# Performance work log

Measured on AMD Instinct MI355X. Metric: run time of the kernel, lower is better.

The kernel has to match this reference:

```python
import jax, jax.numpy as jnp
import numpy as np

NUM_CAPS = 2          # NUM_CLASSES
R = 16 * 10 * 10 * 10 # num_route_nodes = 16000
NUM_ITERS = 3


def conv3d(x, w, b, stride):
    y = jax.lax.conv_general_dilated(
        x, w, window_strides=(stride, stride, stride), padding='VALID',
        dimension_numbers=('NCDHW', 'OIDHW', 'NCDHW'))
    return y + b[None, :, None, None, None]


def squash(t, axis=-1):
    n = jnp.linalg.norm(t, axis=axis, keepdims=True)
    scale = n ** 2 / (1 + n ** 2) / (n + 1e-8)
    return scale * t


def setup_inputs() -> dict:
    key = jax.random.key(0)
    ks = jax.random.split(key, 16)
    inp = {
        'x': jax.random.normal(ks[0], (16, 1, 29, 29, 29), jnp.float32),
        'conv1_w': 0.05 * jax.random.normal(ks[1], (128, 1, 3, 3, 3), jnp.float32),
        'conv1_b': jnp.zeros((128,), jnp.float32),
        # 8 primary capsules, each Conv3d(128,16,k=9,s=2), stacked cap-major
        'pcaps_w': 0.01 * jax.random.normal(ks[2], (8 * 16, 128, 9, 9, 9), jnp.float32),
        'pcaps_b': jnp.zeros((8 * 16,), jnp.float32),
        'route_w': 0.01 * jax.random.normal(ks[3], (NUM_CAPS, R, 8, 16), jnp.float32),
        'dec_w1': 0.05 * jax.random.normal(ks[4], (32, 512), jnp.float32),
        'dec_b1': jnp.zeros((512,), jnp.float32),
        'dec_w2': 0.05 * jax.random.normal(ks[5], (512, 2048), jnp.float32),
        'dec_b2': jnp.zeros((2048,), jnp.float32),
        'dec_w3': 0.02 * jax.random.normal(ks[6], (2048, 10240), jnp.float32),
        'dec_b3': jnp.zeros((10240,), jnp.float32),
        'dec_w4': 0.02 * jax.random.normal(ks[7], (10240, 27000), jnp.float32),
        'dec_b4': jnp.zeros((27000,), jnp.float32),
    }
    return inp


def reference(x, conv1_w, conv1_b, pcaps_w, pcaps_b, route_w,
              dec_w1, dec_b1, dec_w2, dec_b2, dec_w3, dec_b3, dec_w4, dec_b4):
    B = x.shape[0]
    # stem conv + relu: [B,128,27,27,27]
    h = jax.nn.relu(conv3d(x, conv1_w, conv1_b, 1))
    # primary capsules (8 convs fused into one): [B,128,10,10,10]
    p = conv3d(h, pcaps_w, pcaps_b, 2)
    # torch: per-capsule view(B,-1,1) then cat dim=-1 -> [B,16000,8]
    p = p.reshape(B, 8, R).transpose(0, 2, 1)
    u = squash(p, axis=-1)  # [B,R,8]

    # priors: x[:,None,:,None,:] @ W[None] -> [B,C,R,16] (singleton dim dropped)
    priors = jnp.einsum('bri,crio->bcro', u, route_w)
    priors_d = jax.lax.stop_gradient(priors)
    # torch logits have trailing dim 16 but are constant along it (delta is
    # broadcast), so [B,C,R,1] is mathematically identical.
    logits = jnp.zeros((B, NUM_CAPS, R, 1), priors.dtype)

    for i in range(NUM_ITERS):
        probs = jax.nn.softmax(logits, axis=1)  # over capsule axis
        if i == NUM_ITERS - 1:
            v = squash((probs * priors).sum(axis=2, keepdims=True))
        else:
            v = squash((probs * priors_d).sum(axis=2, keepdims=True))
            logits = logits + (priors_d * v).sum(axis=-1, keepdims=True)

    caps = v[:, :, 0, :]  # [B,C,16] (squeeze)
    classes = jnp.linalg.norm(caps, axis=-1)  # [B,C]

    # y=None branch: one-hot of argmax
    y = jax.nn.one_hot(jnp.argmax(classes, axis=1), NUM_CAPS, dtype=caps.dtype)
    d = (caps * y[:, :, None]).reshape(B, -1)  # [B,32]
    d = jax.nn.relu(d @ dec_w1 + dec_b1)
    d = jax.nn.relu(d @ dec_w2 + dec_b2)
    d = jax.nn.relu(d @ dec_w3 + dec_b3)
    recon = jax.nn.sigmoid(d @ dec_w4 + dec_b4)  # [B,27000]
    return classes, recon
```

## Files before the change

kernel.cpp:

```cpp
#include <hip/hip_runtime.h>
#include <hip/hip_bf16.h>

#define NB   16
#define XS   29
#define HS   27
#define HSP  19683
#define PSP  1000
#define RR   16000
#define KTAP 729
#define SPTOT 314928

#define HT_SLOT   81648UL
#define HT_TOTAL  41803776UL
#define HT_PLANE  3024
#define W2B_CH    4096
#define W2B_ICG   376832UL

#define OFF_WT   0UL
#define OFF_H    11943936UL
#define OFF_SP   52254720UL
#define OFF_U    54302720UL
#define OFF_PRI  56350720UL
#define OFF_LOG  64542720UL
#define OFF_V    65055232UL
#define OFF_D0   65055744UL
#define OFF_D1   65056256UL
#define OFF_D2   65064448UL
#define OFF_D3   65097216UL
#define OFF_PP   65693056UL
#define OFF_D3P  82077056UL
#define OFF_D4P  84698496UL

typedef __attribute__((ext_vector_type(8))) short bf16x8;
typedef __attribute__((ext_vector_type(4))) float f32x4;

#define GL2LDS16(g, l) __builtin_amdgcn_global_load_lds( \
    (const __attribute__((address_space(1))) void*)(g), \
    (__attribute__((address_space(3))) void*)(l), 16, 0, 0)

__global__ void prep_w2b(const float* __restrict__ w, ushort* __restrict__ w2b) {
    int gid = blockIdx.x * 256 + threadIdx.x;
    int oc  = gid / 11776;
    int r   = gid % 11776;
    int icg = r / 368;
    int r2  = r % 368;
    int c = r2 >> 2, kq = r2 & 3;
    const float* wb = w + (size_t)oc * 93312 + (size_t)icg * 4 * KTAP;
    ushort vals[8];
    #pragma unroll
    for (int j = 0; j < 8; j++) {
        int ic = j & 3, half = j >> 2;
        float v = 0.f;
        if (c < 81) {
            int tap = c * 9 + 2 * kq + half;
            v = wb[ic * KTAP + tap];
        } else {
            int dzy = (c - 81) * 8 + 2 * kq + half;
            if (dzy <= 80) v = wb[ic * KTAP + dzy * 9 + 8];
        }
        __hip_bfloat16 hv = __float2bfloat16(v);
        vals[j] = *(ushort*)&hv;
    }
    ushort* dst = w2b + ((size_t)((icg * 92 + c) * 4 + kq) * 128 + oc) * 8;
    #pragma unroll
    for (int j = 0; j < 8; j++) dst[j] = vals[j];
}

__global__ __launch_bounds__(256) void conv1_relu_t(const float* __restrict__ x,
                                                    const float* __restrict__ w,
                                                    const float* __restrict__ bias,
                                                    ushort* __restrict__ hT) {
    __shared__ ushort lt[32][132];
    int t = threadIdx.x;
    int c = t & 127;
    float wr[27];
    #pragma unroll
    for (int k = 0; k < 27; k++) wr[k] = w[c * 27 + k];
    float bv = bias[c];
    int sp0 = blockIdx.x * 32;
    #pragma unroll 4
    for (int i = 0; i < 16; i++) {
        int spl = i * 2 + (t >> 7);
        int spg = sp0 + spl;
        if (spg < SPTOT) {
            int b = spg / HSP, sp = spg % HSP;
            int z = sp / 729, y = (sp / 27) % 27, xx = sp % 27;
            const float* xb = x + (size_t)b * (XS * XS * XS) + ((size_t)z * XS + y) * XS + xx;
            float xv[27];
            #pragma unroll
            for (int dz = 0; dz < 3; dz++)
                #pragma unroll
                for (int dy = 0; dy < 3; dy++)
                    #pragma unroll
                    for (int dx = 0; dx < 3; dx++)
                        xv[(dz * 3 + dy) * 3 + dx] = xb[((size_t)dz * XS + dy) * XS + dx];
            float acc = bv;
            #pragma unroll
            for (int k = 0; k < 27; k++) acc = fmaf(xv[k], wr[k], acc);
            __hip_bfloat16 hv = __float2bfloat16(fmaxf(acc, 0.f));
            lt[spl][c] = *(ushort*)&hv;
        }
    }
    __syncthreads();
    #pragma unroll
    for (int q = 0; q < 4; q++) {
        int gidx = q * 256 + t;
        int icg = gidx >> 5, spl = gidx & 31;
        int spg = sp0 + spl;
        if (spg < SPTOT) {
            int b = spg / HSP, sp = spg % HSP;
            int z = sp / 729, y = (sp / 27) % 27, xx = sp % 27;
            *(short4*)(hT + (size_t)(icg * 16 + b) * HT_SLOT
                          + ((size_t)(z * 27 + y) * 28 + xx) * 4) =
                *(const short4*)&lt[spl][icg * 4];
        }
    }
}

__global__ __launch_bounds__(512, 4) void pcaps_conv(const ushort* __restrict__ hT,
                                                     const ushort* __restrict__ w2b,
                                                     float* __restrict__ pp) {
    __shared__ __align__(16) ushort AT[36288];
    int t = threadIdx.x;
    int bid = blockIdx.x;
    int g = bid & 7;
    int rest = bid >> 3;
    int b = rest / 5, ozt = rest % 5;
    int z0 = ozt * 4;

    int lane = t & 63, wave = t >> 6;
    int ocb = wave * 16;
    int l15 = lane & 15, kq = lane >> 4;

    int vox[13];
    #pragma unroll
    for (int f = 0; f < 13; f++) {
        int lr = f * 16 + l15; if (lr > 199) lr = 199;
        int ozl = lr / 100; int rem = lr % 100;
        int oy = rem / 10, ox = rem % 10;
        vox[f] = (2 * ozl) * 6048 + (2 * oy) * 224 + (2 * ox) * 8;
    }

    f32x4 acc[13];
    #pragma unroll
    for (int f = 0; f < 13; f++) acc[f] = (f32x4)0.f;

    int bvoff = (kq * 128 + ocb + l15) * 8;

    for (int ph = 0; ph < 4; ++ph) {
        int icg = g * 4 + ph;
        const ushort* src = hT + (size_t)(icg * 16 + b) * HT_SLOT + (size_t)z0 * HT_PLANE;
        if (ph) __syncthreads();
        #pragma unroll
        for (int q = 0; q < 9; q++) {
            int gi = q * 512 + t;
            if (gi < 4536)
                GL2LDS16(src + (size_t)gi * 8, AT + (size_t)gi * 8);
        }
        asm volatile("s_waitcnt vmcnt(0)" ::: "memory");
        __syncthreads();

        const ushort* wB = w2b + (size_t)icg * W2B_ICG;
        bf16x8 bv = *(const bf16x8*)(wB + bvoff);
        for (int c = 0; c < 81; ++c) {
            bf16x8 bvn = *(const bf16x8*)(wB + (size_t)(c + 1) * W2B_CH + bvoff);
            int coff = (c / 9) * 6048 + (c % 9) * 224 + kq * 16;
            #pragma unroll
            for (int f = 0; f < 13; f++) {
                bf16x8 av = *(const bf16x8*)((const char*)AT + vox[f] + coff);
                acc[f] = __builtin_amdgcn_mfma_f32_16x16x32_bf16(av, bv, acc[f], 0, 0, 0);
            }
            bv = bvn;
        }
        for (int cc = 0; cc < 11; ++cc) {
            int nxt = (cc == 10) ? 91 : 82 + cc;
            bf16x8 bvn = *(const bf16x8*)(wB + (size_t)nxt * W2B_CH + bvoff);
            int dzy0 = cc * 8 + 2 * kq;
            int dzy1 = dzy0 + 1;
            int o0 = (dzy0 / 9) * 6048 + (dzy0 % 9) * 224 + 64;
            int o1 = (dzy1 / 9) * 6048 + (dzy1 % 9) * 224 + 64;
            #pragma unroll
            for (int f = 0; f < 13; f++) {
                union { bf16x8 v; short4 h[2]; } a;
                a.h[0] = *(const short4*)((const char*)AT + vox[f] + o0);
                a.h[1] = *(const short4*)((const char*)AT + vox[f] + o1);
                acc[f] = __builtin_amdgcn_mfma_f32_16x16x32_bf16(a.v, bv, acc[f], 0, 0, 0);
            }
            bv = bvn;
        }
    }

    float* pg = pp + (size_t)g * 2048000;
    int mbase = b * 1000 + ozt * 200;
    #pragma unroll
    for (int f = 0; f < 13; f++) {
        #pragma unroll
        for (int r = 0; r < 4; r++) {
            int lr = f * 16 + kq * 4 + r;
            if (lr < 200)
                pg[(size_t)(mbase + lr) * 128 + ocb + l15] = acc[f][r];
        }
    }
}

__global__ void squash_red(const float* __restrict__ pp, const float* __restrict__ pb,
                           float* __restrict__ u) {
    __shared__ float rowv[2][128];
    int t = threadIdx.x;
    int m = blockIdx.x * 2 + (t >> 7);
    int ch = t & 127;
    float v = pb[ch];
    #pragma unroll
    for (int g = 0; g < 8; g++) v += pp[(size_t)g * 2048000 + (size_t)m * 128 + ch];
    rowv[t >> 7][ch] = v;
    __syncthreads();
    if (t < 32) {
        int row = t >> 4, rq = t & 15;
        int mm = blockIdx.x * 2 + row;
        int b = mm / PSP, s = mm % PSP;
        float vals[8], ss = 0.f;
        #pragma unroll
        for (int i = 0; i < 8; i++) { float x = rowv[row][i * 16 + rq]; vals[i] = x; ss += x * x; }
        float n = sqrtf(ss);
        float sc = ss / (1.f + ss) / (n + 1e-8f);
        float* dst = u + ((size_t)b * RR + rq * 1000 + s) * 8;
        #pragma unroll
        for (int i = 0; i < 8; i++) dst[i] = vals[i] * sc;
    }
}

__global__ void priors_k(const float* __restrict__ u, const float* __restrict__ rw,
                         float* __restrict__ pri) {
    __shared__ float wl[16][132];
    int bx = blockIdx.x; int c = bx / 1000; int r0 = (bx % 1000) * 16;
    int t = threadIdx.x;
    const float4* src = (const float4*)(rw + ((size_t)c * RR + r0) * 128);
    #pragma unroll
    for (int q = 0; q < 8; q++) {
        int idx = q * 256 + t;
        int row = idx >> 5, c4 = idx & 31;
        *(float4*)&wl[row][c4 * 4] = src[idx];
    }
    __syncthreads();
    int bb = t >> 4, rl = t & 15;
    const float* up = u + ((size_t)bb * RR + r0 + rl) * 8;
    float4 u0 = *(const float4*)up, u1 = *(const float4*)(up + 4);
    float uu[8] = {u0.x, u0.y, u0.z, u0.w, u1.x, u1.y, u1.z, u1.w};
    float out[16];
    #pragma unroll
    for (int o = 0; o < 16; o++) out[o] = 0.f;
    #pragma unroll
    for (int i = 0; i < 8; i++)
        #pragma unroll
        for (int o = 0; o < 16; o++) out[o] += uu[i] * wl[rl][i * 16 + o];
    float* dst = pri + ((size_t)(bb * 2 + c) * RR + r0 + rl) * 16;
    #pragma unroll
    for (int q = 0; q < 4; q++)
        *(float4*)&dst[q * 4] = make_float4(out[q*4], out[q*4+1], out[q*4+2], out[q*4+3]);
}

__global__ void route_s0(const float* __restrict__ pri, float* __restrict__ spart) {
    int b = blockIdx.x, chunk = blockIdx.y;
    int t = threadIdx.x, o = t & 15, rl = t >> 4;
    float acc0 = 0.f, acc1 = 0.f;
    for (int j = 0; j < 40; j++) {
        int r = chunk * 640 + j * 16 + rl;
        acc0 += pri[((size_t)(b * 2 + 0) * RR + r) * 16 + o];
        acc1 += pri[((size_t)(b * 2 + 1) * RR + r) * 16 + o];
    }
    __shared__ float red[2][16][17];
    red[0][rl][o] = acc0; red[1][rl][o] = acc1;
    __syncthreads();
    for (int step = 8; step >= 1; step >>= 1) {
        if (rl < step) {
            red[0][rl][o] += red[0][rl + step][o];
            red[1][rl][o] += red[1][rl + step][o];
        }
        __syncthreads();
    }
    if (rl == 0) {
        spart[((b * 25 + chunk) * 2 + 0) * 16 + o] = 0.5f * red[0][0][o];
        spart[((b * 25 + chunk) * 2 + 1) * 16 + o] = 0.5f * red[1][0][o];
    }
}

template<int MODE>
__global__ void route_iter(const float* __restrict__ pri, const float* __restrict__ v,
                           float* __restrict__ lg, float* __restrict__ spart) {
    int b = blockIdx.x, chunk = blockIdx.y;
    int t = threadIdx.x, o = t & 15, rl = t >> 4;
    float v0 = v[(b * 2 + 0) * 16 + o], v1 = v[(b * 2 + 1) * 16 + o];
    float acc0 = 0.f, acc1 = 0.f;
    for (int j = 0; j < 40; j++) {
        int r = chunk * 640 + j * 16 + rl;
        float p0 = pri[((size_t)(b * 2 + 0) * RR + r) * 16 + o];
        float p1 = pri[((size_t)(b * 2 + 1) * RR + r) * 16 + o];
        float d0 = p0 * v0, d1 = p1 * v1;
        #pragma unroll
        for (int w = 1; w < 16; w <<= 1) { d0 += __shfl_xor(d0, w); d1 += __shfl_xor(d1, w); }
        float l0, l1;
        if (MODE == 1) {
            l0 = d0; l1 = d1;
            if (o == 0) lg[(size_t)(b * 2 + 0) * RR + r] = d0;
            if (o == 1) lg[(size_t)(b * 2 + 1) * RR + r] = d1;
        } else {
            l0 = lg[(size_t)(b * 2 + 0) * RR + r] + d0;
            l1 = lg[(size_t)(b * 2 + 1) * RR + r] + d1;
        }
        float mx = fmaxf(l0, l1);
        float e0 = __expf(l0 - mx), e1 = __expf(l1 - mx);
        float inv = 1.f / (e0 + e1);
        acc0 += (e0 * inv) * p0;
        acc1 += (e1 * inv) * p1;
    }
    __shared__ float red[2][16][17];
    red[0][rl][o] = acc0; red[1][rl][o] = acc1;
    __syncthreads();
    for (int step = 8; step >= 1; step >>= 1) {
        if (rl < step) {
            red[0][rl][o] += red[0][rl + step][o];
            red[1][rl][o] += red[1][rl + step][o];
        }
        __syncthreads();
    }
    if (rl == 0) {
        spart[((b * 25 + chunk) * 2 + 0) * 16 + o] = red[0][0][o];
        spart[((b * 25 + chunk) * 2 + 1) * 16 + o] = red[1][0][o];
    }
}

__global__ void squash_v_parts(const float* __restrict__ spart, float* __restrict__ v) {
    int t = threadIdx.x;
    int bc = t >> 4, o = t & 15;
    int b = bc >> 1, c = bc & 1;
    float x = 0.f;
    for (int ch = 0; ch < 25; ch++) x += spart[((b * 25 + ch) * 2 + c) * 16 + o];
    __shared__ float sv[32][17];
    sv[bc][o] = x;
    __syncthreads();
    float ss = 0.f;
    #pragma unroll
    for (int i = 0; i < 16; i++) { float y = sv[bc][i]; ss += y * y; }
    float n = sqrtf(ss);
    float sc = ss / (1.f + ss) / (n + 1e-8f);
    v[bc * 16 + o] = x * sc;
}

__global__ void squash_v_cls(const float* __restrict__ spart, float* __restrict__ out,
                             float* __restrict__ d0) {
    int t = threadIdx.x;
    int bc = t >> 4, o = t & 15;
    int b = bc >> 1, c = bc & 1;
    float x = 0.f;
    for (int ch = 0; ch < 25; ch++) x += spart[((b * 25 + ch) * 2 + c) * 16 + o];
    __shared__ float sv[32][17];
    __shared__ float vv[32][17];
    __shared__ float cls[32];
    sv[bc][o] = x;
    __syncthreads();
    float ss = 0.f;
    #pragma unroll
    for (int i = 0; i < 16; i++) { float y = sv[bc][i]; ss += y * y; }
    float n = sqrtf(ss);
    float sc = ss / (1.f + ss) / (n + 1e-8f);
    vv[bc][o] = x * sc;
    __syncthreads();
    if (t < 32) {
        float s2 = 0.f;
        #pragma unroll
        for (int i = 0; i < 16; i++) { float y = vv[t][i]; s2 += y * y; }
        float nn = sqrtf(s2);
        cls[t] = nn; out[t] = nn;
    }
    __syncthreads();
    int bb = t >> 5, k = t & 31, cc = k >> 4;
    int win = (cls[bb * 2 + 1] > cls[bb * 2 + 0]) ? 1 : 0;
    d0[t] = (cc == win) ? vv[bb * 2 + cc][k & 15] : 0.f;
}

template<int K>
__global__ void dec_small(const float* __restrict__ din, const float* __restrict__ W,
                          const float* __restrict__ bias, float* __restrict__ dout, int N) {
    __shared__ float dl[16 * K];
    int t = threadIdx.x;
    for (int i = t; i < 16 * K; i += 256) dl[i] = din[i];
    __syncthreads();
    int n = blockIdx.x * 256 + t;
    if (n >= N) return;
    float acc[16];
    float bv = bias[n];
    #pragma unroll
    for (int b = 0; b < 16; b++) acc[b] = bv;
    for (int k = 0; k < K; k++) {
        float w = W[(size_t)k * N + n];
        #pragma unroll
        for (int b = 0; b < 16; b++) acc[b] += dl[b * K + k] * w;
    }
    #pragma unroll
    for (int b = 0; b < 16; b++) dout[(size_t)b * N + n] = fmaxf(acc[b], 0.f);
}

__global__ void dec_split(const float* __restrict__ din, const float* __restrict__ W,
                          float* __restrict__ part, int N, int K, int KC) {
    extern __shared__ float dl[];
    int t = threadIdx.x;
    int ky = blockIdx.y;
    int k0 = ky * KC;
    for (int i = t; i < 16 * KC; i += 256) {
        int b = i / KC, kk = i % KC;
        dl[i] = din[(size_t)b * K + k0 + kk];
    }
    __syncthreads();
    int n = blockIdx.x * 1024 + t * 4;
    if (n >= N) return;
    float4 acc[16];
    #pragma unroll
    for (int b = 0; b < 16; b++) acc[b] = make_float4(0.f, 0.f, 0.f, 0.f);
    const float* Wp = W + (size_t)k0 * N + n;
    for (int kk = 0; kk < KC; kk++) {
        float4 w = *(const float4*)&Wp[(size_t)kk * N];
        #pragma unroll
        for (int b = 0; b < 16; b++) {
            float dv = dl[b * KC + kk];
            acc[b].x += dv * w.x; acc[b].y += dv * w.y;
            acc[b].z += dv * w.z; acc[b].w += dv * w.w;
        }
    }
    #pragma unroll
    for (int b = 0; b < 16; b++)
        *(float4*)&part[((size_t)(ky * 16 + b)) * N + n] = acc[b];
}

__global__ void bias_act_sum(const float* __restrict__ part, const float* __restrict__ bias,
                             float* __restrict__ out, int N, int total, int sigm) {
    int gid = blockIdx.x * 256 + threadIdx.x;
    if (gid >= total) return;
    int b = gid / N, n = gid % N;
    float x = bias[n];
    #pragma unroll
    for (int ky = 0; ky < 16; ky++)
        x += part[((size_t)(ky * 16 + b)) * N + n];
    out[gid] = sigm ? (1.f / (1.f + __expf(-x))) : fmaxf(x, 0.f);
}

extern "C" void kernel_launch(void* const* d_in, const int* in_sizes, int n_in,
                              void* d_out, int out_size, void* d_ws, size_t ws_size,
                              hipStream_t stream) {
    const float* x        = (const float*)d_in[0];
    const float* conv1_w  = (const float*)d_in[1];
    const float* conv1_b  = (const float*)d_in[2];
    const float* pcaps_w  = (const float*)d_in[3];
    const float* pcaps_b  = (const float*)d_in[4];
    const float* route_w  = (const float*)d_in[5];
    const float* dec_w1   = (const float*)d_in[6];
    const float* dec_b1   = (const float*)d_in[7];
    const float* dec_w2   = (const float*)d_in[8];
    const float* dec_b2   = (const float*)d_in[9];
    const float* dec_w3   = (const float*)d_in[10];
    const float* dec_b3   = (const float*)d_in[11];
    const float* dec_w4   = (const float*)d_in[12];
    const float* dec_b4   = (const float*)d_in[13];
    float* out = (float*)d_out;

    float* ws = (float*)d_ws;
    ushort* w2b = (ushort*)(ws + OFF_WT);
    ushort* hT  = (ushort*)(ws + OFF_H);
    float* spart = ws + OFF_SP;
    float* u    = ws + OFF_U;
    float* pri  = ws + OFF_PRI;
    float* lg   = ws + OFF_LOG;
    float* v    = ws + OFF_V;
    float* d0   = ws + OFF_D0;
    float* d1   = ws + OFF_D1;
    float* d2   = ws + OFF_D2;
    float* d3   = ws + OFF_D3;
    float* pp   = ws + OFF_PP;
    float* d3p  = ws + OFF_D3P;
    float* d4p  = ws + OFF_D4P;

    prep_w2b<<<5888, 256, 0, stream>>>(pcaps_w, w2b);
    conv1_relu_t<<<9842, 256, 0, stream>>>(x, conv1_w, conv1_b, hT);
    hipMemsetAsync(hT + HT_TOTAL, 0, 8192, stream);

    pcaps_conv<<<640, 512, 0, stream>>>(hT, w2b, pp);
    squash_red<<<8000, 256, 0, stream>>>(pp, pcaps_b, u);

    priors_k<<<2000, 256, 0, stream>>>(u, route_w, pri);

    route_s0<<<dim3(16, 25), 256, 0, stream>>>(pri, spart);
    squash_v_parts<<<1, 512, 0, stream>>>(spart, v);
    route_iter<1><<<dim3(16, 25), 256, 0, stream>>>(pri, v, lg, spart);
    squash_v_parts<<<1, 512, 0, stream>>>(spart, v);
    route_iter<2><<<dim3(16, 25), 256, 0, stream>>>(pri, v, lg, spart);
    squash_v_cls<<<1, 512, 0, stream>>>(spart, out, d0);

    dec_small<32><<<2, 256, 0, stream>>>(d0, dec_w1, dec_b1, d1, 512);
    dec_small<512><<<8, 256, 0, stream>>>(d1, dec_w2, dec_b2, d2, 2048);

    dec_split<<<dim3(10, 16), 256, 16 * 128 * sizeof(float), stream>>>(d2, dec_w3, d3p, 10240, 2048, 128);
    bias_act_sum<<<(16 * 10240 + 255) / 256, 256, 0, stream>>>(d3p, dec_b3, d3, 10240, 16 * 10240, 0);

    dec_split<<<dim3(27, 16), 256, 16 * 640 * sizeof(float), stream>>>(d3, dec_w4, d4p, 27000, 10240, 640);
    bias_act_sum<<<(16 * 27000 + 255) / 256, 256, 0, stream>>>(d4p, dec_b4, out + 32, 27000, 16 * 27000, 1);
}
```

Measured before the change: 1.215 ms.

## Retile pcaps conv waves to 2x32 output tiles and deepen decoder split-K

The primary-capsule conv now gives each wave 32 output channels over half the voxel rows, so every A fragment loaded from LDS feeds two MFMAs. This halves LDS reads per MFMA, though the second B fragment adds extra global weight loads. Separately, the two large decoder GEMMs split K into 32 and 64 chunks instead of 16 to launch more blocks and use more CUs. That makes the partial buffers larger, so the workspace offset is moved and the reduction kernel now takes a variable count of partials.

```diff
diff --git a/kernel.cpp b/kernel.cpp
--- a/kernel.cpp
+++ b/kernel.cpp
@@ -29,7 +29,7 @@
 #define OFF_D3   65097216UL
 #define OFF_PP   65693056UL
 #define OFF_D3P  82077056UL
-#define OFF_D4P  84698496UL
+#define OFF_D4P  87319936UL
 
 typedef __attribute__((ext_vector_type(8))) short bf16x8;
 typedef __attribute__((ext_vector_type(4))) float f32x4;
@@ -129,23 +129,24 @@
     int z0 = ozt * 4;
 
     int lane = t & 63, wave = t >> 6;
-    int ocb = wave * 16;
+    int wo = wave & 3, wm = wave >> 2;
+    int ocb = wo * 32;
     int l15 = lane & 15, kq = lane >> 4;
 
-    int vox[13];
-    #pragma unroll
-    for (int f = 0; f < 13; f++) {
-        int lr = f * 16 + l15; if (lr > 199) lr = 199;
-        int ozl = lr / 100; int rem = lr % 100;
-        int oy = rem / 10, ox = rem % 10;
-        vox[f] = (2 * ozl) * 6048 + (2 * oy) * 224 + (2 * ox) * 8;
-    }
-
-    f32x4 acc[13];
-    #pragma unroll
-    for (int f = 0; f < 13; f++) acc[f] = (f32x4)0.f;
-
-    int bvoff = (kq * 128 + ocb + l15) * 8;
+    int vox[7];
+    #pragma unroll
+    for (int f = 0; f < 7; f++) {
+        int lr = f * 16 + l15; if (lr > 99) lr = 99;
+        int oy = lr / 10, ox = lr % 10;
+        vox[f] = (2 * wm) * 6048 + (2 * oy) * 224 + (2 * ox) * 8;
+    }
+
+    f32x4 acc[7][2];
+    #pragma unroll
+    for (int f = 0; f < 7; f++) { acc[f][0] = (f32x4)0.f; acc[f][1] = (f32x4)0.f; }
+
+    int bvoff0 = (kq * 128 + ocb + l15) * 8;
+    int bvoff1 = bvoff0 + 128;
 
     for (int ph = 0; ph < 4; ++ph) {
         int icg = g * 4 + ph;
@@ -161,44 +162,52 @@
         __syncthreads();
 
         const ushort* wB = w2b + (size_t)icg * W2B_ICG;
-        bf16x8 bv = *(const bf16x8*)(wB + bvoff);
+        bf16x8 bv0 = *(const bf16x8*)(wB + bvoff0);
+        bf16x8 bv1 = *(const bf16x8*)(wB + bvoff1);
         for (int c = 0; c < 81; ++c) {
-            bf16x8 bvn = *(const bf16x8*)(wB + (size_t)(c + 1) * W2B_CH + bvoff);
+            bf16x8 bn0 = *(const bf16x8*)(wB + (size_t)(c + 1) * W2B_CH + bvoff0);
+            bf16x8 bn1 = *(const bf16x8*)(wB + (size_t)(c + 1) * W2B_CH + bvoff1);
             int coff = (c / 9) * 6048 + (c % 9) * 224 + kq * 16;
             #pragma unroll
-            for (int f = 0; f < 13; f++) {
+            for (int f = 0; f < 7; f++) {
                 bf16x8 av = *(const bf16x8*)((const char*)AT + vox[f] + coff);
-                acc[f] = __builtin_amdgcn_mfma_f32_16x16x32_bf16(av, bv, acc[f], 0, 0, 0);
+                acc[f][0] = __builtin_amdgcn_mfma_f32_16x16x32_bf16(av, bv0, acc[f][0], 0, 0, 0);
+                acc[f][1] = __builtin_amdgcn_mfma_f32_16x16x32_bf16(av, bv1, acc[f][1], 0, 0, 0);
             }
-            bv = bvn;
+            bv0 = bn0; bv1 = bn1;
         }
         for (int cc = 0; cc < 11; ++cc) {
             int nxt = (cc == 10) ? 91 : 82 + cc;
-            bf16x8 bvn = *(const bf16x8*)(wB + (size_t)nxt * W2B_CH + bvoff);
+            bf16x8 bn0 = *(const bf16x8*)(wB + (size_t)nxt * W2B_CH + bvoff0);
+            bf16x8 bn1 = *(const bf16x8*)(wB + (size_t)nxt * W2B_CH + bvoff1);
             int dzy0 = cc * 8 + 2 * kq;
             int dzy1 = dzy0 + 1;
             int o0 = (dzy0 / 9) * 6048 + (dzy0 % 9) * 224 + 64;
             int o1 = (dzy1 / 9) * 6048 + (dzy1 % 9) * 224 + 64;
             #pragma unroll
-            for (int f = 0; f < 13; f++) {
+            for (int f = 0; f < 7; f++) {
                 union { bf16x8 v; short4 h[2]; } a;
                 a.h[0] = *(const short4*)((const char*)AT + vox[f] + o0);
                 a.h[1] = *(const short4*)((const char*)AT + vox[f] + o1);
-                acc[f] = __builtin_amdgcn_mfma_f32_16x16x32_bf16(a.v, bv, acc[f], 0, 0, 0);
+                acc[f][0] = __builtin_amdgcn_mfma_f32_16x16x32_bf16(a.v, bv0, acc[f][0], 0, 0, 0);
+                acc[f][1] = __builtin_amdgcn_mfma_f32_16x16x32_bf16(a.v, bv1, acc[f][1], 0, 0, 0);
             }
-            bv = bvn;
+            bv0 = bn0; bv1 = bn1;
         }
     }
 
     float* pg = pp + (size_t)g * 2048000;
-    int mbase = b * 1000 + ozt * 200;
-    #pragma unroll
-    for (int f = 0; f < 13; f++) {
+    int mbase = b * 1000 + ozt * 200 + wm * 100;
+    #pragma unroll
+    for (int f = 0; f < 7; f++) {
         #pragma unroll
         for (int r = 0; r < 4; r++) {
             int lr = f * 16 + kq * 4 + r;
-            if (lr < 200)
-                pg[(size_t)(mbase + lr) * 128 + ocb + l15] = acc[f][r];
+            if (lr < 100) {
+                size_t row = (size_t)(mbase + lr) * 128;
+                pg[row + ocb + l15]      = acc[f][0][r];
+                pg[row + ocb + 16 + l15] = acc[f][1][r];
+            }
         }
     }
 }
@@ -432,13 +441,12 @@
 }
 
 __global__ void bias_act_sum(const float* __restrict__ part, const float* __restrict__ bias,
-                             float* __restrict__ out, int N, int total, int sigm) {
+                             float* __restrict__ out, int N, int total, int sigm, int KY) {
     int gid = blockIdx.x * 256 + threadIdx.x;
     if (gid >= total) return;
     int b = gid / N, n = gid % N;
     float x = bias[n];
-    #pragma unroll
-    for (int ky = 0; ky < 16; ky++)
+    for (int ky = 0; ky < KY; ky++)
         x += part[((size_t)(ky * 16 + b)) * N + n];
     out[gid] = sigm ? (1.f / (1.f + __expf(-x))) : fmaxf(x, 0.f);
 }
@@ -497,9 +505,9 @@
     dec_small<32><<<2, 256, 0, stream>>>(d0, dec_w1, dec_b1, d1, 512);
     dec_small<512><<<8, 256, 0, stream>>>(d1, dec_w2, dec_b2, d2, 2048);
 
-    dec_split<<<dim3(10, 16), 256, 16 * 128 * sizeof(float), stream>>>(d2, dec_w3, d3p, 10240, 2048, 128);
-    bias_act_sum<<<(16 * 10240 + 255) / 256, 256, 0, stream>>>(d3p, dec_b3, d3, 10240, 16 * 10240, 0);
-
-    dec_split<<<dim3(27, 16), 256, 16 * 640 * sizeof(float), stream>>>(d3, dec_w4, d4p, 27000, 10240, 640);
-    bias_act_sum<<<(16 * 27000 + 255) / 256, 256, 0, stream>>>(d4p, dec_b4, out + 32, 27000, 16 * 27000, 1);
-}
+    dec_split<<<dim3(10, 32), 256, 16 * 64 * sizeof(float), stream>>>(d2, dec_w3, d3p, 10240, 2048, 64);
+    bias_act_sum<<<(16 * 10240 + 255) / 256, 256, 0, stream>>>(d3p, dec_b3, d3, 10240, 16 * 10240, 0, 32);
+
+    dec_split<<<dim3(27, 64), 256, 16 * 160 * sizeof(float), stream>>>(d3, dec_w4, d4p, 27000, 10240, 160);
+    bias_act_sum<<<(16 * 27000 + 255) / 256, 256, 0, stream>>>(d4p, dec_b4, out + 32, 27000, 16 * 27000, 1, 64);
+}
```

After: 1.318 ms. 8.5% more time.
